# Kernel tuning notes

Hardware: AMD Instinct MI355X
Metric: run time of the kernel (lower is better)

The kernel has to match this reference:

```python
import math
import jax, jax.numpy as jnp
import numpy as np

E = 8        # num_experts
TOPK = 2     # moe_top_k
CF = 1.25    # capacity_factor
EPS = 1e-5   # LayerNorm eps
NEG = -1e30  # sentinel for masked routing keys


def setup_inputs() -> dict:
    key = jax.random.key(0)
    ks = jax.random.split(key, 8)
    B, S, H, F = 4, 2048, 1024, 4096
    hidden_states = jax.random.normal(ks[0], (B, S, H), jnp.float32)
    token_mask = jnp.ones((B, S), jnp.int32)
    # router: Linear(H -> E), weight init N(0, 0.001), zero bias
    Wr = jax.random.normal(ks[1], (H, E), jnp.float32) * 0.001
    br = jnp.zeros((E,), jnp.float32)
    # per-expert MLP weights stacked along expert axis
    W1 = jax.random.normal(ks[2], (E, H, F), jnp.float32) * (1.0 / np.sqrt(H))
    b1 = jax.random.normal(ks[3], (E, F), jnp.float32) * 0.01
    W2 = jax.random.normal(ks[4], (E, F, H), jnp.float32) * (1.0 / np.sqrt(F))
    b2 = jax.random.normal(ks[5], (E, H), jnp.float32) * 0.01
    gamma = jnp.ones((H,), jnp.float32)
    beta = jnp.zeros((H,), jnp.float32)
    return {"hidden_states": hidden_states, "Wr": Wr, "br": br, "W1": W1,
            "b1": b1, "W2": W2, "b2": b2, "gamma": gamma, "beta": beta,
            "token_mask": token_mask}


def _layer_norm(x, gamma, beta):
    mu = jnp.mean(x, axis=-1, keepdims=True)
    var = jnp.mean((x - mu) ** 2, axis=-1, keepdims=True)
    return (x - mu) * jax.lax.rsqrt(var + EPS) * gamma + beta


def reference(hidden_states, Wr, br, W1, b1, W2, b2, gamma, beta, token_mask):
    # route_mask_pad_tokens=False and jitter=0 -> token_mask ignored, no noise
    B, S, H = hidden_states.shape
    x = hidden_states.reshape(-1, H)              # [N, H]
    N = x.shape[0]
    logits = x @ Wr + br                          # [N, E]
    top_vals, top_idx = jax.lax.top_k(logits, TOPK)  # [N, K]
    w = jax.nn.softmax(top_vals, axis=-1)         # [N, K]

    flat_idx = top_idx.reshape(-1)                # [N*K] expert per assignment
    flat_tok = jnp.repeat(jnp.arange(N), TOPK)    # [N*K] token per assignment
    w_flat = w.reshape(-1)                        # [N*K]

    cap = max(int(math.ceil(N / E * CF)), 1)
    # per-expert keys: weight if assignment routed to e else NEG  -> [E, N*K]
    key_mat = jnp.where(flat_idx[None, :] == jnp.arange(E)[:, None],
                        w_flat[None, :], NEG)
    # keep top-cap assignments by gate weight per expert (capacity drop)
    kv, ki = jax.lax.top_k(key_mat, cap)          # [E, cap]
    valid = kv > NEG / 2                          # real assignments only
    tok = flat_tok[ki]                            # [E, cap] token ids
    gate = jnp.where(valid, w_flat[ki], 0.0)      # [E, cap]

    xe = x[tok]                                   # [E, cap, H] gather
    h1 = jnp.einsum('ech,ehf->ecf', xe, W1) + b1[:, None, :]
    h1 = jax.nn.gelu(h1, approximate=False)       # torch nn.GELU (erf)
    y = jnp.einsum('ecf,efh->ech', h1, W2) + b2[:, None, :]

    out = jnp.zeros_like(x).at[tok.reshape(-1)].add(
        (y * gate[..., None]).reshape(-1, H))     # scatter-add combine
    out = out.reshape(B, S, H) + hidden_states    # residual
    return _layer_norm(out, gamma, beta)
```

## Files before the change

### kernel.cpp

```cpp
#include <hip/hip_runtime.h>
#include <math.h>

#define N_TOK 8192
#define H_DIM 1024
#define E_NUM 8
#define F_DIM 4096
#define CAP   1280
#define NA    (N_TOK*2)
#define KSPLIT 2

typedef short   short8  __attribute__((ext_vector_type(8)));
typedef float   floatx4 __attribute__((ext_vector_type(4)));

__device__ __forceinline__ unsigned short f2b(float f) {
  unsigned u = __float_as_uint(f);
  unsigned r = (u + 0x7fffu + ((u >> 16) & 1u)) >> 16;
  return (unsigned short)r;
}

__device__ __forceinline__ void async_cp16(const void* g, void* l) {
  __builtin_amdgcn_global_load_lds(
      (__attribute__((address_space(1))) void*)(void*)g,
      (__attribute__((address_space(3))) void*)l, 16, 0, 0);
}

__global__ __launch_bounds__(256) void transpose_cvt(const float* __restrict__ src,
                                                     unsigned short* __restrict__ dst,
                                                     int R, int C) {
  __shared__ float tile[64 * 68];
  const int e  = blockIdx.z;
  const int r0 = blockIdx.y * 64, c0 = blockIdx.x * 64;
  const int tid = threadIdx.x;
  const float* s = src + (size_t)e * R * C;
  unsigned short* d = dst + (size_t)e * R * C;
  const int rr = tid >> 4;
  const int c4 = (tid & 15) * 4;
#pragma unroll
  for (int it = 0; it < 4; ++it) {
    const int r = rr + it * 16;
    const float4 v = *(const float4*)(s + (size_t)(r0 + r) * C + c0 + c4);
    *(float4*)(&tile[r * 68 + c4]) = v;
  }
  __syncthreads();
  const int cc = tid >> 3;
  const int r8 = (tid & 7) * 8;
#pragma unroll
  for (int it = 0; it < 2; ++it) {
    const int c = cc + it * 32;
    uint4 u;
    unsigned short* pu = (unsigned short*)&u;
#pragma unroll
    for (int i = 0; i < 8; ++i) pu[i] = f2b(tile[(r8 + i) * 68 + c]);
    *(uint4*)(d + (size_t)(c0 + c) * R + r0 + r8) = u;
  }
}

__global__ __launch_bounds__(256) void router_kernel(const float* __restrict__ x,
                                                     const float* __restrict__ Wr,
                                                     const float* __restrict__ br,
                                                     int* __restrict__ eid,
                                                     float* __restrict__ wf) {
  const int token = blockIdx.x * 4 + (threadIdx.x >> 6);
  const int lane  = threadIdx.x & 63;
  const float* xr = x + (size_t)token * H_DIM;
  float acc[E_NUM];
#pragma unroll
  for (int e = 0; e < E_NUM; ++e) acc[e] = 0.f;
  for (int h = lane; h < H_DIM; h += 64) {
    const float xv = xr[h];
    const float* wr = Wr + h * E_NUM;
#pragma unroll
    for (int e = 0; e < E_NUM; ++e) acc[e] += xv * wr[e];
  }
#pragma unroll
  for (int off = 32; off > 0; off >>= 1) {
#pragma unroll
    for (int e = 0; e < E_NUM; ++e) acc[e] += __shfl_down(acc[e], off, 64);
  }
  if (lane == 0) {
#pragma unroll
    for (int e = 0; e < E_NUM; ++e) acc[e] += br[e];
    int i0 = 0;
#pragma unroll
    for (int e = 1; e < E_NUM; ++e) if (acc[e] > acc[i0]) i0 = e;
    int i1 = (i0 == 0) ? 1 : 0;
    for (int e = 0; e < E_NUM; ++e) if (e != i0 && acc[e] > acc[i1]) i1 = e;
    const float ex = expf(acc[i1] - acc[i0]);
    const float inv = 1.f / (1.f + ex);
    eid[token * 2]     = i0;
    eid[token * 2 + 1] = i1;
    wf[token * 2]      = inv;
    wf[token * 2 + 1]  = ex * inv;
  }
}

#define MAXEQ 4096
__global__ __launch_bounds__(1024) void select_kernel(const int* __restrict__ eid,
                                                      const float* __restrict__ wf,
                                                      int* __restrict__ tok_e,
                                                      float* __restrict__ gate_e) {
  const int e = blockIdx.x;
  const int tid = threadIdx.x;
  __shared__ unsigned hist[256];
  __shared__ unsigned sPrefix, sNeed, sKeepAll, sSlot, eqCnt;
  __shared__ int eq[MAXEQ];
  if (tid == 0) { sPrefix = 0; sNeed = CAP; sKeepAll = 0; sSlot = 0; eqCnt = 0; }
  __syncthreads();
  for (int level = 0; level < 4; ++level) {
    if (tid < 256) hist[tid] = 0;
    __syncthreads();
    const unsigned pref = sPrefix;
    const int shift = 24 - level * 8;
    for (int i = tid; i < NA; i += 1024) {
      if (eid[i] == e) {
        const unsigned wb = __float_as_uint(wf[i]);
        if (level == 0 || (wb >> (shift + 8)) == pref)
          atomicAdd(&hist[(wb >> shift) & 255u], 1u);
      }
    }
    __syncthreads();
    if (tid == 0) {
      const unsigned need = sNeed;
      if (level == 0) {
        unsigned tot = 0;
        for (int b = 0; b < 256; ++b) tot += hist[b];
        if (tot <= (unsigned)CAP) sKeepAll = 1;
      }
      if (!sKeepAll) {
        unsigned cum = 0; int b = 255;
        for (; b > 0; --b) {
          if (cum + hist[b] >= need) break;
          cum += hist[b];
        }
        sPrefix = (sPrefix << 8) | (unsigned)b;
        sNeed = need - cum;
      }
    }
    __syncthreads();
    if (sKeepAll) break;
  }
  const unsigned keepAll = sKeepAll;
  const unsigned thr = sPrefix;
  for (int i = tid; i < NA; i += 1024) {
    if (eid[i] != e) continue;
    const unsigned wb = __float_as_uint(wf[i]);
    if (keepAll || wb > thr) {
      const unsigned s = atomicAdd(&sSlot, 1u);
      tok_e[e * CAP + s]  = i >> 1;
      gate_e[e * CAP + s] = wf[i];
    } else if (wb == thr) {
      const unsigned p = atomicAdd(&eqCnt, 1u);
      if (p < MAXEQ) eq[p] = i;
    }
  }
  __syncthreads();
  if (!keepAll) {
    const int r = (int)sNeed;
    const int t = min((int)eqCnt, MAXEQ);
    for (int a2 = tid; a2 < t; a2 += 1024) {
      const int idx = eq[a2];
      int rank = 0;
      for (int b2 = 0; b2 < t; ++b2) rank += (eq[b2] < idx);
      if (rank < r) {
        const unsigned s = atomicAdd(&sSlot, 1u);
        tok_e[e * CAP + s]  = idx >> 1;
        gate_e[e * CAP + s] = wf[idx];
      }
    }
  }
}

__global__ __launch_bounds__(128) void gather_kernel(const float* __restrict__ x,
                                                     const int* __restrict__ tok_e,
                                                     unsigned short* __restrict__ xe) {
  const int s = blockIdx.x;
  const int t = threadIdx.x;
  const int tok = tok_e[s];
  uint4* dst = (uint4*)(xe + (size_t)s * H_DIM) + t;
  if (tok < 0) { uint4 z; z.x = z.y = z.z = z.w = 0u; *dst = z; return; }
  const float4* xp = (const float4*)x + (size_t)tok * (H_DIM / 4);
  const float4 v0 = xp[t * 2], v1 = xp[t * 2 + 1];
  uint4 u;
  u.x = (unsigned)f2b(v0.x) | ((unsigned)f2b(v0.y) << 16);
  u.y = (unsigned)f2b(v0.z) | ((unsigned)f2b(v0.w) << 16);
  u.z = (unsigned)f2b(v1.x) | ((unsigned)f2b(v1.y) << 16);
  u.w = (unsigned)f2b(v1.z) | ((unsigned)f2b(v1.w) << 16);
  *dst = u;
}

__device__ __forceinline__ void mfma_loop(const unsigned short* Ab,
                                          const unsigned short* Bb,
                                          int kBeg, int kEnd, int ld,
                                          floatx4 acc[4][4],
                                          unsigned short* As, unsigned short* Bs) {
  const int tid  = threadIdx.x;
  const int lane = tid & 63;
  const int w    = tid >> 6;
  const int wm   = (w >> 1) * 64, wn = (w & 1) * 64;
  const int lrow = lane & 15, lk = (lane >> 4) * 8;
  const int r0 = tid >> 2;
  const int c0 = (tid & 3) * 8;
  const int r1 = (tid + 256) >> 2;
  for (int k0 = kBeg; k0 < kEnd; k0 += 32) {
    async_cp16(Ab + (size_t)r0 * ld + k0 + c0, As + tid * 8);
    async_cp16(Ab + (size_t)r1 * ld + k0 + c0, As + (tid + 256) * 8);
    async_cp16(Bb + (size_t)r0 * ld + k0 + c0, Bs + tid * 8);
    async_cp16(Bb + (size_t)r1 * ld + k0 + c0, Bs + (tid + 256) * 8);
    __syncthreads();
    short8 a[4], b[4];
#pragma unroll
    for (int i = 0; i < 4; ++i)
      a[i] = *(const short8*)(As + (wm + i * 16 + lrow) * 32 + lk);
#pragma unroll
    for (int i = 0; i < 4; ++i)
      b[i] = *(const short8*)(Bs + (wn + i * 16 + lrow) * 32 + lk);
#pragma unroll
    for (int mi = 0; mi < 4; ++mi)
#pragma unroll
      for (int ni = 0; ni < 4; ++ni)
        acc[mi][ni] = __builtin_amdgcn_mfma_f32_16x16x32_bf16(a[mi], b[ni], acc[mi][ni], 0, 0, 0);
    __syncthreads();
  }
}

__global__ __launch_bounds__(256) void gemm1_kernel(const unsigned short* __restrict__ xe,
                                                    const unsigned short* __restrict__ WT,
                                                    const float* __restrict__ b1,
                                                    unsigned short* __restrict__ h1) {
  __shared__ unsigned short As[128 * 32], Bs[128 * 32];
  const int e  = blockIdx.z;
  const int m0 = blockIdx.y * 128, n0 = blockIdx.x * 128;
  const unsigned short* Ab = xe + ((size_t)e * CAP + m0) * H_DIM;
  const unsigned short* Bb = WT + ((size_t)e * F_DIM + n0) * H_DIM;
  floatx4 acc[4][4];
#pragma unroll
  for (int mi = 0; mi < 4; ++mi)
#pragma unroll
    for (int ni = 0; ni < 4; ++ni) acc[mi][ni] = (floatx4){0.f, 0.f, 0.f, 0.f};
  mfma_loop(Ab, Bb, 0, H_DIM, H_DIM, acc, As, Bs);
  const int lane = threadIdx.x & 63, w = threadIdx.x >> 6;
  const int wm = (w >> 1) * 64, wn = (w & 1) * 64;
  const int col0  = n0 + wn + (lane & 15);
  const int rbase = m0 + wm + ((lane >> 4) * 4);
#pragma unroll
  for (int ni = 0; ni < 4; ++ni) {
    const int col = col0 + ni * 16;
    const float bias = b1[e * F_DIM + col];
#pragma unroll
    for (int mi = 0; mi < 4; ++mi) {
#pragma unroll
      for (int j = 0; j < 4; ++j) {
        const int row = rbase + mi * 16 + j;
        float v = acc[mi][ni][j] + bias;
        v = 0.5f * v * (1.0f + erff(v * 0.70710678118654752f));
        h1[((size_t)e * CAP + row) * F_DIM + col] = f2b(v);
      }
    }
  }
}

__global__ __launch_bounds__(256) void gemm2_kernel(const unsigned short* __restrict__ h1,
                                                    const unsigned short* __restrict__ WT,
                                                    const float* __restrict__ b2,
                                                    const int* __restrict__ tok_e,
                                                    const float* __restrict__ gate_e,
                                                    float* __restrict__ out) {
  __shared__ unsigned short As[128 * 32], Bs[128 * 32];
  const int z  = blockIdx.z;
  const int e  = z >> 1;
  const int kc = z & 1;
  const int m0 = blockIdx.y * 128, n0 = blockIdx.x * 128;
  const unsigned short* Ab = h1 + ((size_t)e * CAP + m0) * F_DIM;
  const unsigned short* Bb = WT + ((size_t)e * H_DIM + n0) * F_DIM;
  floatx4 acc[4][4];
#pragma unroll
  for (int mi = 0; mi < 4; ++mi)
#pragma unroll
    for (int ni = 0; ni < 4; ++ni) acc[mi][ni] = (floatx4){0.f, 0.f, 0.f, 0.f};
  const int kLen = F_DIM / KSPLIT;
  mfma_loop(Ab, Bb, kc * kLen, kc * kLen + kLen, F_DIM, acc, As, Bs);
  const int lane = threadIdx.x & 63, w = threadIdx.x >> 6;
  const int wm = (w >> 1) * 64, wn = (w & 1) * 64;
  const int col0  = n0 + wn + (lane & 15);
  const int rbase = m0 + wm + ((lane >> 4) * 4);
  float b2v[4];
#pragma unroll
  for (int ni = 0; ni < 4; ++ni)
    b2v[ni] = (kc == 0) ? b2[e * H_DIM + col0 + ni * 16] : 0.f;
#pragma unroll
  for (int mi = 0; mi < 4; ++mi) {
#pragma unroll
    for (int j = 0; j < 4; ++j) {
      const int row = rbase + mi * 16 + j;
      const int tok = tok_e[e * CAP + row];
      if (tok < 0) continue;
      const float g = gate_e[e * CAP + row];
      float* orow = out + (size_t)tok * H_DIM;
#pragma unroll
      for (int ni = 0; ni < 4; ++ni) {
        const float v = acc[mi][ni][j] + b2v[ni];
        atomicAdd(orow + col0 + ni * 16, g * v);
      }
    }
  }
}

__global__ __launch_bounds__(256) void ln_kernel(float* __restrict__ out,
                                                 const float* __restrict__ gamma,
                                                 const float* __restrict__ beta) {
  const int token = blockIdx.x;
  const int tid = threadIdx.x;
  const int lane = tid & 63, w = tid >> 6;
  float* row = out + (size_t)token * H_DIM;
  float v[4];
#pragma unroll
  for (int i = 0; i < 4; ++i) v[i] = row[tid + i * 256];
  float s = v[0] + v[1] + v[2] + v[3];
  __shared__ float red[8];
#pragma unroll
  for (int off = 32; off > 0; off >>= 1) s += __shfl_down(s, off, 64);
  if (lane == 0) red[w] = s;
  __syncthreads();
  const float mu = (red[0] + red[1] + red[2] + red[3]) * (1.f / H_DIM);
  float q = 0.f;
#pragma unroll
  for (int i = 0; i < 4; ++i) { const float d = v[i] - mu; q += d * d; }
#pragma unroll
  for (int off = 32; off > 0; off >>= 1) q += __shfl_down(q, off, 64);
  if (lane == 0) red[4 + w] = q;
  __syncthreads();
  const float var = (red[4] + red[5] + red[6] + red[7]) * (1.f / H_DIM);
  const float rs = rsqrtf(var + 1e-5f);
#pragma unroll
  for (int i = 0; i < 4; ++i) {
    const int h = tid + i * 256;
    row[h] = (v[i] - mu) * rs * gamma[h] + beta[h];
  }
}

extern "C" void kernel_launch(void* const* d_in, const int* in_sizes, int n_in,
                              void* d_out, int out_size, void* d_ws, size_t ws_size,
                              hipStream_t stream) {
  const float* x     = (const float*)d_in[0];
  const float* Wr    = (const float*)d_in[1];
  const float* br    = (const float*)d_in[2];
  const float* W1    = (const float*)d_in[3];
  const float* b1    = (const float*)d_in[4];
  const float* W2    = (const float*)d_in[5];
  const float* b2    = (const float*)d_in[6];
  const float* gamma = (const float*)d_in[7];
  const float* beta  = (const float*)d_in[8];
  float* out = (float*)d_out;

  char* ws = (char*)d_ws;
  unsigned short* WT   = (unsigned short*)(ws);
  unsigned short* xe   = (unsigned short*)(ws + 67108864);
  unsigned short* h1   = (unsigned short*)(ws + 88080384);
  int*            eid  = (int*)(ws + 171966464);
  float*          wf   = (float*)(ws + 172032000);
  int*            tok_e  = (int*)(ws + 172097536);
  float*          gate_e = (float*)(ws + 172138496);

  transpose_cvt<<<dim3(F_DIM / 64, H_DIM / 64, E_NUM), 256, 0, stream>>>(W1, WT, H_DIM, F_DIM);
  router_kernel<<<N_TOK / 4, 256, 0, stream>>>(x, Wr, br, eid, wf);
  hipMemsetAsync(tok_e, 0xFF, E_NUM * CAP * sizeof(int), stream);
  hipMemsetAsync(gate_e, 0, E_NUM * CAP * sizeof(float), stream);
  select_kernel<<<E_NUM, 1024, 0, stream>>>(eid, wf, tok_e, gate_e);
  gather_kernel<<<E_NUM * CAP, 128, 0, stream>>>(x, tok_e, xe);
  gemm1_kernel<<<dim3(F_DIM / 128, CAP / 128, E_NUM), 256, 0, stream>>>(xe, WT, b1, h1);
  transpose_cvt<<<dim3(H_DIM / 64, F_DIM / 64, E_NUM), 256, 0, stream>>>(W2, WT, F_DIM, H_DIM);
  hipMemcpyAsync(out, x, (size_t)N_TOK * H_DIM * sizeof(float), hipMemcpyDeviceToDevice, stream);
  gemm2_kernel<<<dim3(H_DIM / 128, CAP / 128, E_NUM * KSPLIT), 256, 0, stream>>>(h1, WT, b2, tok_e, gate_e, out);
  ln_kernel<<<N_TOK, 256, 0, stream>>>(out, gamma, beta);
}
```

Before: 756.1 us.

## Replace atomic scatter-add combine with per-slot output and fused combine+LayerNorm

The second expert GEMM now writes plain per-slot outputs y with bias instead of split-K atomics into the output. A new combine_ln kernel gathers each token's two expert rows through a slot_of map built in select_kernel, adds the gated results to the residual and applies LayerNorm in one pass. This removes the device-to-device residual copy, the float atomics and the KSPLIT split. The cost is a 40MB fp32 y buffer and fewer gemm2 blocks (no split-K), which may reduce occupancy. The new path only runs when the workspace is large enough, otherwise a non-split atomic fallback is used.

```diff
diff --git a/kernel.cpp b/kernel.cpp
--- a/kernel.cpp
+++ b/kernel.cpp
@@ -7,7 +7,6 @@
 #define F_DIM 4096
 #define CAP   1280
 #define NA    (N_TOK*2)
-#define KSPLIT 2
 
 typedef short   short8  __attribute__((ext_vector_type(8)));
 typedef float   floatx4 __attribute__((ext_vector_type(4)));
@@ -98,7 +97,8 @@
 __global__ __launch_bounds__(1024) void select_kernel(const int* __restrict__ eid,
                                                       const float* __restrict__ wf,
                                                       int* __restrict__ tok_e,
-                                                      float* __restrict__ gate_e) {
+                                                      float* __restrict__ gate_e,
+                                                      int* __restrict__ slot_of) {
   const int e = blockIdx.x;
   const int tid = threadIdx.x;
   __shared__ unsigned hist[256];
@@ -148,6 +148,7 @@
       const unsigned s = atomicAdd(&sSlot, 1u);
       tok_e[e * CAP + s]  = i >> 1;
       gate_e[e * CAP + s] = wf[i];
+      if (slot_of) slot_of[i] = e * CAP + (int)s;
     } else if (wb == thr) {
       const unsigned p = atomicAdd(&eqCnt, 1u);
       if (p < MAXEQ) eq[p] = i;
@@ -165,6 +166,7 @@
         const unsigned s = atomicAdd(&sSlot, 1u);
         tok_e[e * CAP + s]  = idx >> 1;
         gate_e[e * CAP + s] = wf[idx];
+        if (slot_of) slot_of[idx] = e * CAP + (int)s;
       }
     }
   }
@@ -190,7 +192,7 @@
 
 __device__ __forceinline__ void mfma_loop(const unsigned short* Ab,
                                           const unsigned short* Bb,
-                                          int kBeg, int kEnd, int ld,
+                                          int Kdim, int ld,
                                           floatx4 acc[4][4],
                                           unsigned short* As, unsigned short* Bs) {
   const int tid  = threadIdx.x;
@@ -201,7 +203,7 @@
   const int r0 = tid >> 2;
   const int c0 = (tid & 3) * 8;
   const int r1 = (tid + 256) >> 2;
-  for (int k0 = kBeg; k0 < kEnd; k0 += 32) {
+  for (int k0 = 0; k0 < Kdim; k0 += 32) {
     async_cp16(Ab + (size_t)r0 * ld + k0 + c0, As + tid * 8);
     async_cp16(Ab + (size_t)r1 * ld + k0 + c0, As + (tid + 256) * 8);
     async_cp16(Bb + (size_t)r0 * ld + k0 + c0, Bs + tid * 8);
@@ -237,7 +239,7 @@
   for (int mi = 0; mi < 4; ++mi)
 #pragma unroll
     for (int ni = 0; ni < 4; ++ni) acc[mi][ni] = (floatx4){0.f, 0.f, 0.f, 0.f};
-  mfma_loop(Ab, Bb, 0, H_DIM, H_DIM, acc, As, Bs);
+  mfma_loop(Ab, Bb, H_DIM, H_DIM, acc, As, Bs);
   const int lane = threadIdx.x & 63, w = threadIdx.x >> 6;
   const int wm = (w >> 1) * 64, wn = (w & 1) * 64;
   const int col0  = n0 + wn + (lane & 15);
@@ -259,16 +261,12 @@
   }
 }
 
-__global__ __launch_bounds__(256) void gemm2_kernel(const unsigned short* __restrict__ h1,
-                                                    const unsigned short* __restrict__ WT,
-                                                    const float* __restrict__ b2,
-                                                    const int* __restrict__ tok_e,
-                                                    const float* __restrict__ gate_e,
-                                                    float* __restrict__ out) {
+__global__ __launch_bounds__(256) void gemm2_y_kernel(const unsigned short* __restrict__ h1,
+                                                      const unsigned short* __restrict__ WT,
+                                                      const float* __restrict__ b2,
+                                                      float* __restrict__ y) {
   __shared__ unsigned short As[128 * 32], Bs[128 * 32];
-  const int z  = blockIdx.z;
-  const int e  = z >> 1;
-  const int kc = z & 1;
+  const int e  = blockIdx.z;
   const int m0 = blockIdx.y * 128, n0 = blockIdx.x * 128;
   const unsigned short* Ab = h1 + ((size_t)e * CAP + m0) * F_DIM;
   const unsigned short* Bb = WT + ((size_t)e * H_DIM + n0) * F_DIM;
@@ -277,16 +275,51 @@
   for (int mi = 0; mi < 4; ++mi)
 #pragma unroll
     for (int ni = 0; ni < 4; ++ni) acc[mi][ni] = (floatx4){0.f, 0.f, 0.f, 0.f};
-  const int kLen = F_DIM / KSPLIT;
-  mfma_loop(Ab, Bb, kc * kLen, kc * kLen + kLen, F_DIM, acc, As, Bs);
+  mfma_loop(Ab, Bb, F_DIM, F_DIM, acc, As, Bs);
   const int lane = threadIdx.x & 63, w = threadIdx.x >> 6;
   const int wm = (w >> 1) * 64, wn = (w & 1) * 64;
   const int col0  = n0 + wn + (lane & 15);
   const int rbase = m0 + wm + ((lane >> 4) * 4);
   float b2v[4];
 #pragma unroll
-  for (int ni = 0; ni < 4; ++ni)
-    b2v[ni] = (kc == 0) ? b2[e * H_DIM + col0 + ni * 16] : 0.f;
+  for (int ni = 0; ni < 4; ++ni) b2v[ni] = b2[e * H_DIM + col0 + ni * 16];
+#pragma unroll
+  for (int mi = 0; mi < 4; ++mi) {
+#pragma unroll
+    for (int j = 0; j < 4; ++j) {
+      const int row = rbase + mi * 16 + j;
+      float* yr = y + ((size_t)e * CAP + row) * H_DIM;
+#pragma unroll
+      for (int ni = 0; ni < 4; ++ni)
+        yr[col0 + ni * 16] = acc[mi][ni][j] + b2v[ni];
+    }
+  }
+}
+
+__global__ __launch_bounds__(256) void gemm2_atomic_kernel(const unsigned short* __restrict__ h1,
+                                                           const unsigned short* __restrict__ WT,
+                                                           const float* __restrict__ b2,
+                                                           const int* __restrict__ tok_e,
+                                                           const float* __restrict__ gate_e,
+                                                           float* __restrict__ out) {
+  __shared__ unsigned short As[128 * 32], Bs[128 * 32];
+  const int e  = blockIdx.z;
+  const int m0 = blockIdx.y * 128, n0 = blockIdx.x * 128;
+  const unsigned short* Ab = h1 + ((size_t)e * CAP + m0) * F_DIM;
+  const unsigned short* Bb = WT + ((size_t)e * H_DIM + n0) * F_DIM;
+  floatx4 acc[4][4];
+#pragma unroll
+  for (int mi = 0; mi < 4; ++mi)
+#pragma unroll
+    for (int ni = 0; ni < 4; ++ni) acc[mi][ni] = (floatx4){0.f, 0.f, 0.f, 0.f};
+  mfma_loop(Ab, Bb, F_DIM, F_DIM, acc, As, Bs);
+  const int lane = threadIdx.x & 63, w = threadIdx.x >> 6;
+  const int wm = (w >> 1) * 64, wn = (w & 1) * 64;
+  const int col0  = n0 + wn + (lane & 15);
+  const int rbase = m0 + wm + ((lane >> 4) * 4);
+  float b2v[4];
+#pragma unroll
+  for (int ni = 0; ni < 4; ++ni) b2v[ni] = b2[e * H_DIM + col0 + ni * 16];
 #pragma unroll
   for (int mi = 0; mi < 4; ++mi) {
 #pragma unroll
@@ -302,6 +335,54 @@
         atomicAdd(orow + col0 + ni * 16, g * v);
       }
     }
+  }
+}
+
+__global__ __launch_bounds__(256) void combine_ln_kernel(const float* __restrict__ x,
+                                                         const float* __restrict__ y,
+                                                         const int* __restrict__ slot_of,
+                                                         const float* __restrict__ wf,
+                                                         const float* __restrict__ gamma,
+                                                         const float* __restrict__ beta,
+                                                         float* __restrict__ out) {
+  const int token = blockIdx.x;
+  const int tid = threadIdx.x;
+  const int lane = tid & 63, w = tid >> 6;
+  const int s0 = slot_of[token * 2], s1 = slot_of[token * 2 + 1];
+  const float g0 = wf[token * 2], g1 = wf[token * 2 + 1];
+  const float* xr = x + (size_t)token * H_DIM;
+  const float* y0 = y + (size_t)(s0 < 0 ? 0 : s0) * H_DIM;
+  const float* y1 = y + (size_t)(s1 < 0 ? 0 : s1) * H_DIM;
+  float v[4];
+#pragma unroll
+  for (int i = 0; i < 4; ++i) {
+    const int h = tid + i * 256;
+    float a = xr[h];
+    if (s0 >= 0) a += g0 * y0[h];
+    if (s1 >= 0) a += g1 * y1[h];
+    v[i] = a;
+  }
+  float s = v[0] + v[1] + v[2] + v[3];
+  __shared__ float red[8];
+#pragma unroll
+  for (int off = 32; off > 0; off >>= 1) s += __shfl_down(s, off, 64);
+  if (lane == 0) red[w] = s;
+  __syncthreads();
+  const float mu = (red[0] + red[1] + red[2] + red[3]) * (1.f / H_DIM);
+  float q = 0.f;
+#pragma unroll
+  for (int i = 0; i < 4; ++i) { const float d = v[i] - mu; q += d * d; }
+#pragma unroll
+  for (int off = 32; off > 0; off >>= 1) q += __shfl_down(q, off, 64);
+  if (lane == 0) red[4 + w] = q;
+  __syncthreads();
+  const float var = (red[4] + red[5] + red[6] + red[7]) * (1.f / H_DIM);
+  const float rs = rsqrtf(var + 1e-5f);
+  float* orow = out + (size_t)token * H_DIM;
+#pragma unroll
+  for (int i = 0; i < 4; ++i) {
+    const int h = tid + i * 256;
+    orow[h] = (v[i] - mu) * rs * gamma[h] + beta[h];
   }
 }
 
@@ -360,16 +441,27 @@
   float*          wf   = (float*)(ws + 172032000);
   int*            tok_e  = (int*)(ws + 172097536);
   float*          gate_e = (float*)(ws + 172138496);
+  int*            slot_of = (int*)(ws + 172179456);
+  float*          y    = (float*)(ws + 172244992);
+  const int use_y = (ws_size >= (size_t)214188032);
+  const int have_slot = (ws_size >= (size_t)172244992);
 
   transpose_cvt<<<dim3(F_DIM / 64, H_DIM / 64, E_NUM), 256, 0, stream>>>(W1, WT, H_DIM, F_DIM);
   router_kernel<<<N_TOK / 4, 256, 0, stream>>>(x, Wr, br, eid, wf);
   hipMemsetAsync(tok_e, 0xFF, E_NUM * CAP * sizeof(int), stream);
   hipMemsetAsync(gate_e, 0, E_NUM * CAP * sizeof(float), stream);
-  select_kernel<<<E_NUM, 1024, 0, stream>>>(eid, wf, tok_e, gate_e);
+  if (have_slot) hipMemsetAsync(slot_of, 0xFF, NA * sizeof(int), stream);
+  select_kernel<<<E_NUM, 1024, 0, stream>>>(eid, wf, tok_e, gate_e,
+                                            have_slot ? slot_of : (int*)nullptr);
   gather_kernel<<<E_NUM * CAP, 128, 0, stream>>>(x, tok_e, xe);
   gemm1_kernel<<<dim3(F_DIM / 128, CAP / 128, E_NUM), 256, 0, stream>>>(xe, WT, b1, h1);
   transpose_cvt<<<dim3(H_DIM / 64, F_DIM / 64, E_NUM), 256, 0, stream>>>(W2, WT, F_DIM, H_DIM);
-  hipMemcpyAsync(out, x, (size_t)N_TOK * H_DIM * sizeof(float), hipMemcpyDeviceToDevice, stream);
-  gemm2_kernel<<<dim3(H_DIM / 128, CAP / 128, E_NUM * KSPLIT), 256, 0, stream>>>(h1, WT, b2, tok_e, gate_e, out);
-  ln_kernel<<<N_TOK, 256, 0, stream>>>(out, gamma, beta);
-}
+  if (use_y) {
+    gemm2_y_kernel<<<dim3(H_DIM / 128, CAP / 128, E_NUM), 256, 0, stream>>>(h1, WT, b2, y);
+    combine_ln_kernel<<<N_TOK, 256, 0, stream>>>(x, y, slot_of, wf, gamma, beta, out);
+  } else {
+    hipMemcpyAsync(out, x, (size_t)N_TOK * H_DIM * sizeof(float), hipMemcpyDeviceToDevice, stream);
+    gemm2_atomic_kernel<<<dim3(H_DIM / 128, CAP / 128, E_NUM), 256, 0, stream>>>(h1, WT, b2, tok_e, gate_e, out);
+    ln_kernel<<<N_TOK, 256, 0, stream>>>(out, gamma, beta);
+  }
+}
```

Result: faster. 712.9 us (-5.7%).
